# Performance work log

Measured on AMD Instinct MI355X. Metric: run time of the kernel, lower is better.

Reference implementation:

```python
import jax, jax.numpy as jnp
import numpy as np

N_NODES = 100000


def gcn_layer(x, src, dst, W, b):
    """PyG GCNConv: add self-loops, symmetric deg normalization, XW then scatter-add."""
    n = x.shape[0]
    loop = jnp.arange(n, dtype=src.dtype)
    s = jnp.concatenate([src, loop])
    d = jnp.concatenate([dst, loop])
    # degree of target nodes (includes self-loop)
    deg = jax.ops.segment_sum(jnp.ones_like(d, dtype=x.dtype), d, num_segments=n)
    dinv = jnp.where(deg > 0, jax.lax.rsqrt(deg), 0.0)
    norm = dinv[s] * dinv[d]                      # [E+N]
    h = x @ W                                     # [N, out]
    msg = h[s] * norm[:, None]                    # [E+N, out]
    out = jax.ops.segment_sum(msg, d, num_segments=n) + b
    return out


def setup_inputs() -> dict:
    key = jax.random.key(0)
    k1, k2, k3, k4 = jax.random.split(key, 4)
    d_in, d_hid, d_out = 256, 256, 128
    E = 3200000
    x = jax.random.normal(k1, (N_NODES, d_in), dtype=jnp.float32)
    edge_index = jax.random.randint(k2, (2, E), 0, N_NODES, dtype=jnp.int64)
    # glorot-style init for GCN weights
    W1 = jax.random.normal(k3, (d_in, d_hid), dtype=jnp.float32) / np.sqrt(d_in)
    b1 = jnp.zeros((d_hid,), dtype=jnp.float32)
    W2 = jax.random.normal(k4, (d_hid, d_out), dtype=jnp.float32) / np.sqrt(d_hid)
    b2 = jnp.zeros((d_out,), dtype=jnp.float32)
    return {"x": x, "W1": W1, "b1": b1, "W2": W2, "b2": b2, "edge_index": edge_index}


def reference(x, W1, b1, W2, b2, edge_index):
    src, dst = edge_index[0], edge_index[1]
    h = jax.nn.relu(gcn_layer(x, src, dst, W1, b1))
    out = jax.nn.relu(gcn_layer(h, src, dst, W2, b2))
    return out
```

## Files before the change

### kernel.cpp

```cpp
#include <hip/hip_runtime.h>


typedef short          s16x8 __attribute__((ext_vector_type(8)));
typedef float          f32x4 __attribute__((ext_vector_type(4)));
typedef unsigned short u16x8 __attribute__((ext_vector_type(8)));
typedef unsigned short u16x4 __attribute__((ext_vector_type(4)));

__device__ __forceinline__ float bf2f(unsigned short u) {
  union { unsigned int i; float f; } x; x.i = ((unsigned int)u) << 16; return x.f;
}
__device__ __forceinline__ unsigned short f2bf(float f) {
  union { float f; unsigned int i; } x; x.f = f;
  unsigned int r = x.i + 0x7FFFu + ((x.i >> 16) & 1u);
  return (unsigned short)(r >> 16);
}


#define NBUCK_PAD 1024
#define BIN_CHUNK 4096

__global__ __launch_bounds__(256) void k_hist(const int* __restrict__ dst,
                                              int* __restrict__ bcnt, int E) {
  __shared__ int h[NBUCK_PAD];
  int t = threadIdx.x;
  for (int i = t; i < NBUCK_PAD; i += 256) h[i] = 0;
  __syncthreads();
  int n4 = E >> 2;
  int stride = gridDim.x * 256;
  const int4* d4 = (const int4*)dst;
  for (int e = blockIdx.x * 256 + t; e < n4; e += stride) {
    int4 v = d4[e];
    atomicAdd(&h[v.x >> 7], 1);
    atomicAdd(&h[v.y >> 7], 1);
    atomicAdd(&h[v.z >> 7], 1);
    atomicAdd(&h[v.w >> 7], 1);
  }
  if (blockIdx.x == 0) {
    for (int e = n4 * 4 + t; e < E; e += 256) atomicAdd(&h[dst[e] >> 7], 1);
  }
  __syncthreads();
  for (int i = t; i < NBUCK_PAD; i += 256) {
    int v = h[i];
    if (v) atomicAdd(bcnt + i, v);
  }
}

__global__ void k_bscan(const int* __restrict__ bcnt, int* __restrict__ bptr,
                        int* __restrict__ bcur, int* __restrict__ rowptr, int M, int E) {
  __shared__ int sh[NBUCK_PAD];
  int t = threadIdx.x;
  int v = bcnt[t];
  sh[t] = v; __syncthreads();
  int x = v;
  for (int off = 1; off < NBUCK_PAD; off <<= 1) {
    int y = (t >= off) ? sh[t - off] : 0;
    __syncthreads();
    x += y; sh[t] = x;
    __syncthreads();
  }
  bptr[t] = x - v;
  bcur[t] = x - v;
  if (t == NBUCK_PAD - 1) bptr[NBUCK_PAD] = x;
  if (t == 0) rowptr[M] = E;
}

__global__ __launch_bounds__(256) void k_bin(const int* __restrict__ src,
                                             const int* __restrict__ dst,
                                             int* __restrict__ bcur,
                                             unsigned int* __restrict__ binned, int E) {
  __shared__ int hist[NBUCK_PAD];
  __shared__ int base[NBUCK_PAD];
  int t = threadIdx.x;
  int e0 = blockIdx.x * BIN_CHUNK;
  int e1 = min(e0 + BIN_CHUNK, E);
  for (int i = t; i < NBUCK_PAD; i += 256) hist[i] = 0;
  __syncthreads();
  for (int e = e0 + t; e < e1; e += 256) atomicAdd(&hist[dst[e] >> 7], 1);
  __syncthreads();
  for (int i = t; i < NBUCK_PAD; i += 256) {
    int h = hist[i];
    base[i] = h ? atomicAdd(bcur + i, h) : 0;
    hist[i] = 0;
  }
  __syncthreads();
  for (int e = e0 + t; e < e1; e += 256) {
    int d = dst[e], s = src[e];
    int b = d >> 7;
    int p = base[b] + atomicAdd(&hist[b], 1);
    binned[p] = ((unsigned)(d & 127) << 17) | (unsigned)s;
  }
}

__global__ __launch_bounds__(256) void k_csr(const unsigned int* __restrict__ binned,
                                             const int* __restrict__ bptr,
                                             int* __restrict__ rowptr,
                                             float* __restrict__ dinv,
                                             int* __restrict__ col, int M) {
  __shared__ int deg[128];
  __shared__ int sc[128];
  __shared__ int cur[128];
  int b = blockIdx.x, t = threadIdx.x;
  int n0 = b << 7;
  int nn = min(128, M - n0);
  int e0 = bptr[b], e1 = bptr[b + 1];
  if (t < 128) deg[t] = 0;
  __syncthreads();
  for (int e = e0 + t; e < e1; e += 256) atomicAdd(&deg[(binned[e] >> 17) & 127], 1);
  __syncthreads();
  if (t < 128) sc[t] = deg[t];
  __syncthreads();
  for (int off = 1; off < 128; off <<= 1) {
    int y = 0;
    if (t < 128 && t >= off) y = sc[t - off];
    __syncthreads();
    if (t < 128) sc[t] += y;
    __syncthreads();
  }
  if (t < nn) {
    int excl = sc[t] - deg[t];
    rowptr[n0 + t] = e0 + excl;
    dinv[n0 + t] = rsqrtf((float)(deg[t] + 1));
    cur[t] = excl;
  }
  __syncthreads();
  for (int e = e0 + t; e < e1; e += 256) {
    unsigned v = binned[e];
    int dl = (v >> 17) & 127;
    int p = e0 + atomicAdd(&cur[dl], 1);
    col[p] = (int)(v & 0x1FFFFu);
  }
}


__global__ void k_cvt_w(const float* __restrict__ W1, const float* __restrict__ W2,
                        unsigned short* __restrict__ w1t, unsigned short* __restrict__ w2t) {
  int i = blockIdx.x * 256 + threadIdx.x;
  if (i < 256 * 256) {
    int k = i >> 8, n = i & 255;
    w1t[n * 256 + k] = f2bf(W1[i]);
  } else {
    int j = i - 256 * 256;
    if (j < 256 * 128) {
      int k = j >> 7, n = j & 127;
      w2t[n * 256 + k] = f2bf(W2[j]);
    }
  }
}


__device__ __forceinline__ int swz4(int row, int kc) { return kc ^ ((row & 3) << 3); }

__global__ __launch_bounds__(512) void k_gemm1(
    const float* __restrict__ X, const unsigned short* __restrict__ Bt,
    const float* __restrict__ dinv, unsigned short* __restrict__ G, int M) {
  const int K = 256;
  __shared__ short lA[128 * 32];
  __shared__ short lB[256 * 32];
  int tid = threadIdx.x;
  int wid = tid >> 6, lane = tid & 63;
  int wm = wid >> 2, wn = wid & 3;
  int l15 = lane & 15;
  int lkg = (lane >> 4) * 8;
  int bm = blockIdx.x * 128;

  f32x4 acc[4][4] = {};

  for (int kt = 0; kt < 8; ++kt) {
    int k0 = kt * 32;
    __syncthreads();
#pragma unroll
    for (int h = 0; h < 2; ++h) {
      int cid = tid + h * 512;
      int r = cid >> 3, c4 = (cid & 7) * 4;
      int gr = bm + r;
      float4 v = {0.f, 0.f, 0.f, 0.f};
      if (gr < M) v = *(const float4*)(X + (size_t)gr * K + k0 + c4);
      u16x4 o; o[0] = f2bf(v.x); o[1] = f2bf(v.y); o[2] = f2bf(v.z); o[3] = f2bf(v.w);
      *(u16x4*)(&lA[r * 32 + swz4(r, c4)]) = o;
    }
#pragma unroll
    for (int h = 0; h < 2; ++h) {
      int cid = tid + h * 512;
      int n = cid >> 2, kc = (cid & 3) * 8;
      s16x8 v = *(const s16x8*)(Bt + (size_t)n * K + k0 + kc);
      *(s16x8*)(&lB[n * 32 + swz4(n, kc)]) = v;
    }
    __syncthreads();

    s16x8 af[4], bfr[4];
#pragma unroll
    for (int mi = 0; mi < 4; ++mi) {
      int r = wm * 64 + mi * 16 + l15;
      af[mi] = *(const s16x8*)(&lA[r * 32 + swz4(r, lkg)]);
    }
#pragma unroll
    for (int ni = 0; ni < 4; ++ni) {
      int c = wn * 64 + ni * 16 + l15;
      bfr[ni] = *(const s16x8*)(&lB[c * 32 + swz4(c, lkg)]);
    }
#pragma unroll
    for (int mi = 0; mi < 4; ++mi)
#pragma unroll
      for (int ni = 0; ni < 4; ++ni)
        acc[mi][ni] = __builtin_amdgcn_mfma_f32_16x16x32_bf16(af[mi], bfr[ni], acc[mi][ni], 0, 0, 0);
  }

#pragma unroll
  for (int mi = 0; mi < 4; ++mi) {
    int mrow0 = bm + wm * 64 + mi * 16 + (lane >> 4) * 4;
#pragma unroll
    for (int j = 0; j < 4; ++j) {
      int m = mrow0 + j;
      if (m < M) {
        float dv = dinv[m];
#pragma unroll
        for (int ni = 0; ni < 4; ++ni)
          G[(size_t)(wn >> 1) * M * 128 + (size_t)m * 128 + (wn & 1) * 64 + ni * 16 + l15]
              = f2bf(acc[mi][ni][j] * dv);
      }
    }
  }
}


__global__ __launch_bounds__(512) void k_gemm2(
    const unsigned short* __restrict__ A, const unsigned short* __restrict__ Bt,
    const float* __restrict__ dinv, unsigned short* __restrict__ G, int M) {
  const int K = 256;
  __shared__ short lA[128 * 32];
  __shared__ short lB[128 * 32];
  int tid = threadIdx.x;
  int wid = tid >> 6, lane = tid & 63;
  int wm = wid >> 2, wn = wid & 3;
  int l15 = lane & 15;
  int lkg = (lane >> 4) * 8;
  int bm = blockIdx.x * 128;

  f32x4 acc[4][2] = {};

  for (int kt = 0; kt < 8; ++kt) {
    int k0 = kt * 32;
    __syncthreads();
    {
      int r = tid >> 2, kc = (tid & 3) * 8;
      int gr = bm + r;
      s16x8 v = {0, 0, 0, 0, 0, 0, 0, 0};
      if (gr < M) v = *(const s16x8*)(A + (size_t)gr * K + k0 + kc);
      *(s16x8*)(&lA[r * 32 + swz4(r, kc)]) = v;
    }
    {
      int n = tid >> 2, kc = (tid & 3) * 8;
      s16x8 v = *(const s16x8*)(Bt + (size_t)n * K + k0 + kc);
      *(s16x8*)(&lB[n * 32 + swz4(n, kc)]) = v;
    }
    __syncthreads();

    s16x8 af[4], bfr[2];
#pragma unroll
    for (int mi = 0; mi < 4; ++mi) {
      int r = wm * 64 + mi * 16 + l15;
      af[mi] = *(const s16x8*)(&lA[r * 32 + swz4(r, lkg)]);
    }
#pragma unroll
    for (int ni = 0; ni < 2; ++ni) {
      int c = wn * 32 + ni * 16 + l15;
      bfr[ni] = *(const s16x8*)(&lB[c * 32 + swz4(c, lkg)]);
    }
#pragma unroll
    for (int mi = 0; mi < 4; ++mi)
#pragma unroll
      for (int ni = 0; ni < 2; ++ni)
        acc[mi][ni] = __builtin_amdgcn_mfma_f32_16x16x32_bf16(af[mi], bfr[ni], acc[mi][ni], 0, 0, 0);
  }

#pragma unroll
  for (int mi = 0; mi < 4; ++mi) {
    int mrow0 = bm + wm * 64 + mi * 16 + (lane >> 4) * 4;
#pragma unroll
    for (int j = 0; j < 4; ++j) {
      int m = mrow0 + j;
      if (m < M) {
        float dv = dinv[m];
#pragma unroll
        for (int ni = 0; ni < 2; ++ni)
          G[(size_t)(wn >> 1) * M * 64 + (size_t)m * 64 + (wn & 1) * 32 + ni * 16 + l15]
              = f2bf(acc[mi][ni][j] * dv);
      }
    }
  }
}


__global__ __launch_bounds__(256) void k_agg256h(
    const unsigned short* __restrict__ G, const int* __restrict__ rowptr,
    const int* __restrict__ col, const float* __restrict__ dinv,
    const float* __restrict__ bias, unsigned short* __restrict__ H,
    int M, int phase) {
  int lane = threadIdx.x & 63;
  int v = (blockIdx.x << 2) + (threadIdx.x >> 6);
  if (v >= M) return;
  int slot = lane >> 4;
  int f8 = (lane & 15) * 8;
  float a[8] = {};
  if (slot == 0) {
    u16x8 s = *(const u16x8*)(G + (size_t)v * 128 + f8);
#pragma unroll
    for (int i = 0; i < 8; ++i) a[i] += bf2f(s[i]);
  }
  int jb = rowptr[v], je = rowptr[v + 1];
  int j = jb;
  for (; j + 8 <= je; j += 8) {
    int u0 = col[j + slot];
    int u1 = col[j + 4 + slot];
    u16x8 p0 = *(const u16x8*)(G + (size_t)u0 * 128 + f8);
    u16x8 p1 = *(const u16x8*)(G + (size_t)u1 * 128 + f8);
#pragma unroll
    for (int i = 0; i < 8; ++i) a[i] += bf2f(p0[i]) + bf2f(p1[i]);
  }
  for (; j + 4 <= je; j += 4) {
    int u = col[j + slot];
    u16x8 p = *(const u16x8*)(G + (size_t)u * 128 + f8);
#pragma unroll
    for (int i = 0; i < 8; ++i) a[i] += bf2f(p[i]);
  }
  int rem = je - j;
  if (slot < rem) {
    int u = col[j + slot];
    u16x8 p = *(const u16x8*)(G + (size_t)u * 128 + f8);
#pragma unroll
    for (int i = 0; i < 8; ++i) a[i] += bf2f(p[i]);
  }
#pragma unroll
  for (int i = 0; i < 8; ++i) {
    a[i] += __shfl_xor(a[i], 16, 64);
    a[i] += __shfl_xor(a[i], 32, 64);
  }
  if (lane < 16) {
    float dv = dinv[v];
    const float* bp = bias + phase * 128 + f8;
    u16x8 o;
#pragma unroll
    for (int i = 0; i < 8; ++i) o[i] = f2bf(fmaxf(fmaf(dv, a[i], bp[i]), 0.f));
    *(u16x8*)(H + (size_t)v * 256 + phase * 128 + f8) = o;
  }
}


__global__ __launch_bounds__(256) void k_agg128h(
    const unsigned short* __restrict__ G, const int* __restrict__ rowptr,
    const int* __restrict__ col, const float* __restrict__ dinv,
    const float* __restrict__ bias, float* __restrict__ Out,
    int M, int phase) {
  int lane = threadIdx.x & 63;
  int v = (blockIdx.x << 2) + (threadIdx.x >> 6);
  if (v >= M) return;
  int slot = lane >> 3;
  int f8 = (lane & 7) * 8;
  float a[8] = {};
  if (slot == 0) {
    u16x8 s = *(const u16x8*)(G + (size_t)v * 64 + f8);
#pragma unroll
    for (int i = 0; i < 8; ++i) a[i] += bf2f(s[i]);
  }
  int jb = rowptr[v], je = rowptr[v + 1];
  int j = jb;
  for (; j + 16 <= je; j += 16) {
    int u0 = col[j + slot];
    int u1 = col[j + 8 + slot];
    u16x8 p0 = *(const u16x8*)(G + (size_t)u0 * 64 + f8);
    u16x8 p1 = *(const u16x8*)(G + (size_t)u1 * 64 + f8);
#pragma unroll
    for (int i = 0; i < 8; ++i) a[i] += bf2f(p0[i]) + bf2f(p1[i]);
  }
  for (; j + 8 <= je; j += 8) {
    int u = col[j + slot];
    u16x8 p = *(const u16x8*)(G + (size_t)u * 64 + f8);
#pragma unroll
    for (int i = 0; i < 8; ++i) a[i] += bf2f(p[i]);
  }
  int rem = je - j;
  if (slot < rem) {
    int u = col[j + slot];
    u16x8 p = *(const u16x8*)(G + (size_t)u * 64 + f8);
#pragma unroll
    for (int i = 0; i < 8; ++i) a[i] += bf2f(p[i]);
  }
#pragma unroll
  for (int i = 0; i < 8; ++i) {
    a[i] += __shfl_xor(a[i], 8, 64);
    a[i] += __shfl_xor(a[i], 16, 64);
    a[i] += __shfl_xor(a[i], 32, 64);
  }
  if (lane < 8) {
    float dv = dinv[v];
    const float* bp = bias + phase * 64 + f8;
    float4 r0, r1;
    r0.x = fmaxf(fmaf(dv, a[0], bp[0]), 0.f);
    r0.y = fmaxf(fmaf(dv, a[1], bp[1]), 0.f);
    r0.z = fmaxf(fmaf(dv, a[2], bp[2]), 0.f);
    r0.w = fmaxf(fmaf(dv, a[3], bp[3]), 0.f);
    r1.x = fmaxf(fmaf(dv, a[4], bp[4]), 0.f);
    r1.y = fmaxf(fmaf(dv, a[5], bp[5]), 0.f);
    r1.z = fmaxf(fmaf(dv, a[6], bp[6]), 0.f);
    r1.w = fmaxf(fmaf(dv, a[7], bp[7]), 0.f);
    float* op = Out + (size_t)v * 128 + phase * 64 + f8;
    *(float4*)op = r0;
    *(float4*)(op + 4) = r1;
  }
}


extern "C" void kernel_launch(void* const* d_in, const int* in_sizes, int n_in,
                              void* d_out, int out_size, void* d_ws, size_t ws_size,
                              hipStream_t stream) {
  const float* x  = (const float*)d_in[0];
  const float* W1 = (const float*)d_in[1];
  const float* b1 = (const float*)d_in[2];
  const float* W2 = (const float*)d_in[3];
  const float* b2 = (const float*)d_in[4];
  const int*   ei = (const int*)d_in[5];

  const int D_IN = 256, D_HID = 256, D_OUT = 128;
  const int M = in_sizes[0] / D_IN;
  const int E = in_sizes[5] / 2;
  const int* src = ei;
  const int* dst = ei + E;

  char* p = (char*)d_ws;
  auto alloc = [&](size_t bytes) { void* r = (void*)p; p += (bytes + 255) & ~(size_t)255; return r; };
  float* dinv = (float*)alloc((size_t)M * 4);
  int* rowptr = (int*)alloc((size_t)(M + 1) * 4);
  int* bcnt   = (int*)alloc(NBUCK_PAD * 4);
  int* bptr   = (int*)alloc((NBUCK_PAD + 1) * 4);
  int* bcur   = (int*)alloc(NBUCK_PAD * 4);
  int* colx   = (int*)alloc((size_t)E * 4);
  unsigned short* w1t = (unsigned short*)alloc((size_t)D_HID * D_IN * 2);
  unsigned short* w2t = (unsigned short*)alloc((size_t)D_OUT * D_HID * 2);
  unsigned short* g1  = (unsigned short*)alloc((size_t)M * D_HID * 2);
  unsigned short* hid = (unsigned short*)alloc((size_t)M * D_HID * 2);
  unsigned short* g2  = (unsigned short*)alloc((size_t)M * D_OUT * 2);
  unsigned int* binned = (unsigned int*)g1;

  int nbuck = (M + 127) >> 7;
  int nbin  = (E + BIN_CHUNK - 1) / BIN_CHUNK;
  int nb4   = (M + 3) / 4;

  hipMemsetAsync(bcnt, 0, NBUCK_PAD * 4, stream);
  k_hist <<<256, 256, 0, stream>>>(dst, bcnt, E);
  k_bscan<<<1, NBUCK_PAD, 0, stream>>>(bcnt, bptr, bcur, rowptr, M, E);
  k_bin  <<<nbin, 256, 0, stream>>>(src, dst, bcur, binned, E);
  k_csr  <<<nbuck, 256, 0, stream>>>(binned, bptr, rowptr, dinv, colx, M);

  k_cvt_w<<<(256 * 256 + 256 * 128 + 255) / 256, 256, 0, stream>>>(W1, W2, w1t, w2t);

  k_gemm1  <<<nbuck, 512, 0, stream>>>(x, w1t, dinv, g1, M);
  k_agg256h<<<nb4, 256, 0, stream>>>(g1,                      rowptr, colx, dinv, b1, hid, M, 0);
  k_agg256h<<<nb4, 256, 0, stream>>>(g1 + (size_t)M * 128,    rowptr, colx, dinv, b1, hid, M, 1);
  k_gemm2  <<<nbuck, 512, 0, stream>>>(hid, w2t, dinv, g2, M);
  k_agg128h<<<nb4, 256, 0, stream>>>(g2,                      rowptr, colx, dinv, b2, (float*)d_out, M, 0);
  k_agg128h<<<nb4, 256, 0, stream>>>(g2 + (size_t)M * 64,     rowptr, colx, dinv, b2, (float*)d_out, M, 1);
}
```

Measured before the change: 540.3 us.

## Merge half-width aggregation passes into single full-row gathers with packed bf16 accumulation

The GEMM outputs now go to contiguous full rows (512B / 256B) instead of two column-half planes. Each aggregation layer therefore runs as one kernel that reads the CSR adjacency once, rather than two half-width passes that each re-read rowptr and col. bf16 pairs are unpacked and accumulated as float2 vectors, which may map to packed FP32 adds. The edge-binning chunk size and histogram grid size are also retuned. The trade-off is fewer neighbours in flight per wave for the 256-wide layer, and working sets that may be less cache-friendly per pass.

```diff
diff --git a/kernel.cpp b/kernel.cpp
--- a/kernel.cpp
+++ b/kernel.cpp
@@ -3,6 +3,7 @@
 
 typedef short          s16x8 __attribute__((ext_vector_type(8)));
 typedef float          f32x4 __attribute__((ext_vector_type(4)));
+typedef float          f32x2 __attribute__((ext_vector_type(2)));
 typedef unsigned short u16x8 __attribute__((ext_vector_type(8)));
 typedef unsigned short u16x4 __attribute__((ext_vector_type(4)));
 
@@ -14,10 +15,17 @@
   unsigned int r = x.i + 0x7FFFu + ((x.i >> 16) & 1u);
   return (unsigned short)(r >> 16);
 }
+__device__ __forceinline__ void acc2(f32x2& a, unsigned int pair) {
+  union { unsigned int u; float f; } lo, hi;
+  lo.u = pair << 16;
+  hi.u = pair & 0xFFFF0000u;
+  f32x2 v = {lo.f, hi.f};
+  a += v;
+}
 
 
 #define NBUCK_PAD 1024
-#define BIN_CHUNK 4096
+#define BIN_CHUNK 32768
 
 __global__ __launch_bounds__(256) void k_hist(const int* __restrict__ dst,
                                               int* __restrict__ bcnt, int E) {
@@ -215,8 +223,7 @@
         float dv = dinv[m];
 #pragma unroll
         for (int ni = 0; ni < 4; ++ni)
-          G[(size_t)(wn >> 1) * M * 128 + (size_t)m * 128 + (wn & 1) * 64 + ni * 16 + l15]
-              = f2bf(acc[mi][ni][j] * dv);
+          G[(size_t)m * 256 + wn * 64 + ni * 16 + l15] = f2bf(acc[mi][ni][j] * dv);
       }
     }
   }
@@ -283,127 +290,125 @@
         float dv = dinv[m];
 #pragma unroll
         for (int ni = 0; ni < 2; ++ni)
-          G[(size_t)(wn >> 1) * M * 64 + (size_t)m * 64 + (wn & 1) * 32 + ni * 16 + l15]
-              = f2bf(acc[mi][ni][j] * dv);
+          G[(size_t)m * 128 + wn * 32 + ni * 16 + l15] = f2bf(acc[mi][ni][j] * dv);
       }
     }
   }
 }
 
 
-__global__ __launch_bounds__(256) void k_agg256h(
+__global__ __launch_bounds__(256) void k_agg256(
     const unsigned short* __restrict__ G, const int* __restrict__ rowptr,
     const int* __restrict__ col, const float* __restrict__ dinv,
-    const float* __restrict__ bias, unsigned short* __restrict__ H,
-    int M, int phase) {
+    const float* __restrict__ bias, unsigned short* __restrict__ H, int M) {
+  int lane = threadIdx.x & 63;
+  int v = (blockIdx.x << 2) + (threadIdx.x >> 6);
+  if (v >= M) return;
+  int slot = lane >> 5;
+  int l32 = lane & 31;
+  int boff = l32 * 16;
+  const char* Gb = (const char*)G;
+  f32x2 a[4] = {};
+  if (slot == 0) {
+    uint4 w = *(const uint4*)(Gb + (((unsigned)v) << 9) + boff);
+    acc2(a[0], w.x); acc2(a[1], w.y); acc2(a[2], w.z); acc2(a[3], w.w);
+  }
+  int jb = rowptr[v], je = rowptr[v + 1];
+  int j = jb;
+  for (; j + 4 <= je; j += 4) {
+    unsigned u0 = (unsigned)col[j + slot];
+    unsigned u1 = (unsigned)col[j + 2 + slot];
+    uint4 w0 = *(const uint4*)(Gb + (u0 << 9) + boff);
+    uint4 w1 = *(const uint4*)(Gb + (u1 << 9) + boff);
+    acc2(a[0], w0.x); acc2(a[1], w0.y); acc2(a[2], w0.z); acc2(a[3], w0.w);
+    acc2(a[0], w1.x); acc2(a[1], w1.y); acc2(a[2], w1.z); acc2(a[3], w1.w);
+  }
+  for (; j + 2 <= je; j += 2) {
+    unsigned u = (unsigned)col[j + slot];
+    uint4 w = *(const uint4*)(Gb + (u << 9) + boff);
+    acc2(a[0], w.x); acc2(a[1], w.y); acc2(a[2], w.z); acc2(a[3], w.w);
+  }
+  if (j < je && slot == 0) {
+    unsigned u = (unsigned)col[j];
+    uint4 w = *(const uint4*)(Gb + (u << 9) + boff);
+    acc2(a[0], w.x); acc2(a[1], w.y); acc2(a[2], w.z); acc2(a[3], w.w);
+  }
+#pragma unroll
+  for (int k = 0; k < 4; ++k) {
+    a[k].x += __shfl_xor(a[k].x, 32, 64);
+    a[k].y += __shfl_xor(a[k].y, 32, 64);
+  }
+  if (slot == 0) {
+    float dv = dinv[v];
+    const float* bp = bias + l32 * 8;
+    u16x8 o;
+#pragma unroll
+    for (int k = 0; k < 4; ++k) {
+      o[2 * k]     = f2bf(fmaxf(fmaf(dv, a[k].x, bp[2 * k]),     0.f));
+      o[2 * k + 1] = f2bf(fmaxf(fmaf(dv, a[k].y, bp[2 * k + 1]), 0.f));
+    }
+    *(u16x8*)(H + (size_t)v * 256 + l32 * 8) = o;
+  }
+}
+
+
+__global__ __launch_bounds__(256) void k_agg128(
+    const unsigned short* __restrict__ G, const int* __restrict__ rowptr,
+    const int* __restrict__ col, const float* __restrict__ dinv,
+    const float* __restrict__ bias, float* __restrict__ Out, int M) {
   int lane = threadIdx.x & 63;
   int v = (blockIdx.x << 2) + (threadIdx.x >> 6);
   if (v >= M) return;
   int slot = lane >> 4;
-  int f8 = (lane & 15) * 8;
-  float a[8] = {};
+  int l16 = lane & 15;
+  int boff = l16 * 16;
+  const char* Gb = (const char*)G;
+  f32x2 a[4] = {};
   if (slot == 0) {
-    u16x8 s = *(const u16x8*)(G + (size_t)v * 128 + f8);
-#pragma unroll
-    for (int i = 0; i < 8; ++i) a[i] += bf2f(s[i]);
+    uint4 w = *(const uint4*)(Gb + (((unsigned)v) << 8) + boff);
+    acc2(a[0], w.x); acc2(a[1], w.y); acc2(a[2], w.z); acc2(a[3], w.w);
   }
   int jb = rowptr[v], je = rowptr[v + 1];
   int j = jb;
   for (; j + 8 <= je; j += 8) {
-    int u0 = col[j + slot];
-    int u1 = col[j + 4 + slot];
-    u16x8 p0 = *(const u16x8*)(G + (size_t)u0 * 128 + f8);
-    u16x8 p1 = *(const u16x8*)(G + (size_t)u1 * 128 + f8);
-#pragma unroll
-    for (int i = 0; i < 8; ++i) a[i] += bf2f(p0[i]) + bf2f(p1[i]);
+    unsigned u0 = (unsigned)col[j + slot];
+    unsigned u1 = (unsigned)col[j + 4 + slot];
+    uint4 w0 = *(const uint4*)(Gb + (u0 << 8) + boff);
+    uint4 w1 = *(const uint4*)(Gb + (u1 << 8) + boff);
+    acc2(a[0], w0.x); acc2(a[1], w0.y); acc2(a[2], w0.z); acc2(a[3], w0.w);
+    acc2(a[0], w1.x); acc2(a[1], w1.y); acc2(a[2], w1.z); acc2(a[3], w1.w);
   }
   for (; j + 4 <= je; j += 4) {
-    int u = col[j + slot];
-    u16x8 p = *(const u16x8*)(G + (size_t)u * 128 + f8);
-#pragma unroll
-    for (int i = 0; i < 8; ++i) a[i] += bf2f(p[i]);
+    unsigned u = (unsigned)col[j + slot];
+    uint4 w = *(const uint4*)(Gb + (u << 8) + boff);
+    acc2(a[0], w.x); acc2(a[1], w.y); acc2(a[2], w.z); acc2(a[3], w.w);
   }
   int rem = je - j;
   if (slot < rem) {
-    int u = col[j + slot];
-    u16x8 p = *(const u16x8*)(G + (size_t)u * 128 + f8);
-#pragma unroll
-    for (int i = 0; i < 8; ++i) a[i] += bf2f(p[i]);
-  }
-#pragma unroll
-  for (int i = 0; i < 8; ++i) {
-    a[i] += __shfl_xor(a[i], 16, 64);
-    a[i] += __shfl_xor(a[i], 32, 64);
-  }
-  if (lane < 16) {
+    unsigned u = (unsigned)col[j + slot];
+    uint4 w = *(const uint4*)(Gb + (u << 8) + boff);
+    acc2(a[0], w.x); acc2(a[1], w.y); acc2(a[2], w.z); acc2(a[3], w.w);
+  }
+#pragma unroll
+  for (int k = 0; k < 4; ++k) {
+    a[k].x += __shfl_xor(a[k].x, 16, 64);
+    a[k].y += __shfl_xor(a[k].y, 16, 64);
+    a[k].x += __shfl_xor(a[k].x, 32, 64);
+    a[k].y += __shfl_xor(a[k].y, 32, 64);
+  }
+  if (slot == 0) {
     float dv = dinv[v];
-    const float* bp = bias + phase * 128 + f8;
-    u16x8 o;
-#pragma unroll
-    for (int i = 0; i < 8; ++i) o[i] = f2bf(fmaxf(fmaf(dv, a[i], bp[i]), 0.f));
-    *(u16x8*)(H + (size_t)v * 256 + phase * 128 + f8) = o;
-  }
-}
-
-
-__global__ __launch_bounds__(256) void k_agg128h(
-    const unsigned short* __restrict__ G, const int* __restrict__ rowptr,
-    const int* __restrict__ col, const float* __restrict__ dinv,
-    const float* __restrict__ bias, float* __restrict__ Out,
-    int M, int phase) {
-  int lane = threadIdx.x & 63;
-  int v = (blockIdx.x << 2) + (threadIdx.x >> 6);
-  if (v >= M) return;
-  int slot = lane >> 3;
-  int f8 = (lane & 7) * 8;
-  float a[8] = {};
-  if (slot == 0) {
-    u16x8 s = *(const u16x8*)(G + (size_t)v * 64 + f8);
-#pragma unroll
-    for (int i = 0; i < 8; ++i) a[i] += bf2f(s[i]);
-  }
-  int jb = rowptr[v], je = rowptr[v + 1];
-  int j = jb;
-  for (; j + 16 <= je; j += 16) {
-    int u0 = col[j + slot];
-    int u1 = col[j + 8 + slot];
-    u16x8 p0 = *(const u16x8*)(G + (size_t)u0 * 64 + f8);
-    u16x8 p1 = *(const u16x8*)(G + (size_t)u1 * 64 + f8);
-#pragma unroll
-    for (int i = 0; i < 8; ++i) a[i] += bf2f(p0[i]) + bf2f(p1[i]);
-  }
-  for (; j + 8 <= je; j += 8) {
-    int u = col[j + slot];
-    u16x8 p = *(const u16x8*)(G + (size_t)u * 64 + f8);
-#pragma unroll
-    for (int i = 0; i < 8; ++i) a[i] += bf2f(p[i]);
-  }
-  int rem = je - j;
-  if (slot < rem) {
-    int u = col[j + slot];
-    u16x8 p = *(const u16x8*)(G + (size_t)u * 64 + f8);
-#pragma unroll
-    for (int i = 0; i < 8; ++i) a[i] += bf2f(p[i]);
-  }
-#pragma unroll
-  for (int i = 0; i < 8; ++i) {
-    a[i] += __shfl_xor(a[i], 8, 64);
-    a[i] += __shfl_xor(a[i], 16, 64);
-    a[i] += __shfl_xor(a[i], 32, 64);
-  }
-  if (lane < 8) {
-    float dv = dinv[v];
-    const float* bp = bias + phase * 64 + f8;
+    const float* bp = bias + l16 * 8;
     float4 r0, r1;
-    r0.x = fmaxf(fmaf(dv, a[0], bp[0]), 0.f);
-    r0.y = fmaxf(fmaf(dv, a[1], bp[1]), 0.f);
-    r0.z = fmaxf(fmaf(dv, a[2], bp[2]), 0.f);
-    r0.w = fmaxf(fmaf(dv, a[3], bp[3]), 0.f);
-    r1.x = fmaxf(fmaf(dv, a[4], bp[4]), 0.f);
-    r1.y = fmaxf(fmaf(dv, a[5], bp[5]), 0.f);
-    r1.z = fmaxf(fmaf(dv, a[6], bp[6]), 0.f);
-    r1.w = fmaxf(fmaf(dv, a[7], bp[7]), 0.f);
-    float* op = Out + (size_t)v * 128 + phase * 64 + f8;
+    r0.x = fmaxf(fmaf(dv, a[0].x, bp[0]), 0.f);
+    r0.y = fmaxf(fmaf(dv, a[0].y, bp[1]), 0.f);
+    r0.z = fmaxf(fmaf(dv, a[1].x, bp[2]), 0.f);
+    r0.w = fmaxf(fmaf(dv, a[1].y, bp[3]), 0.f);
+    r1.x = fmaxf(fmaf(dv, a[2].x, bp[4]), 0.f);
+    r1.y = fmaxf(fmaf(dv, a[2].y, bp[5]), 0.f);
+    r1.z = fmaxf(fmaf(dv, a[3].x, bp[6]), 0.f);
+    r1.w = fmaxf(fmaf(dv, a[3].y, bp[7]), 0.f);
+    float* op = Out + (size_t)v * 128 + l16 * 8;
     *(float4*)op = r0;
     *(float4*)(op + 4) = r1;
   }
@@ -446,17 +451,15 @@
   int nb4   = (M + 3) / 4;
 
   hipMemsetAsync(bcnt, 0, NBUCK_PAD * 4, stream);
-  k_hist <<<256, 256, 0, stream>>>(dst, bcnt, E);
+  k_hist <<<104, 256, 0, stream>>>(dst, bcnt, E);
   k_bscan<<<1, NBUCK_PAD, 0, stream>>>(bcnt, bptr, bcur, rowptr, M, E);
   k_bin  <<<nbin, 256, 0, stream>>>(src, dst, bcur, binned, E);
   k_csr  <<<nbuck, 256, 0, stream>>>(binned, bptr, rowptr, dinv, colx, M);
 
   k_cvt_w<<<(256 * 256 + 256 * 128 + 255) / 256, 256, 0, stream>>>(W1, W2, w1t, w2t);
 
-  k_gemm1  <<<nbuck, 512, 0, stream>>>(x, w1t, dinv, g1, M);
-  k_agg256h<<<nb4, 256, 0, stream>>>(g1,                      rowptr, colx, dinv, b1, hid, M, 0);
-  k_agg256h<<<nb4, 256, 0, stream>>>(g1 + (size_t)M * 128,    rowptr, colx, dinv, b1, hid, M, 1);
-  k_gemm2  <<<nbuck, 512, 0, stream>>>(hid, w2t, dinv, g2, M);
-  k_agg128h<<<nb4, 256, 0, stream>>>(g2,                      rowptr, colx, dinv, b2, (float*)d_out, M, 0);
-  k_agg128h<<<nb4, 256, 0, stream>>>(g2 + (size_t)M * 64,     rowptr, colx, dinv, b2, (float*)d_out, M, 1);
-}
+  k_gemm1 <<<nbuck, 512, 0, stream>>>(x, w1t, dinv, g1, M);
+  k_agg256<<<nb4, 256, 0, stream>>>(g1, rowptr, colx, dinv, b1, hid, M);
+  k_gemm2 <<<nbuck, 512, 0, stream>>>(hid, w2t, dinv, g2, M);
+  k_agg128<<<nb4, 256, 0, stream>>>(g2, rowptr, colx, dinv, b2, (float*)d_out, M);
+}
```

Result: slower. 552.1 us (+2.2%).
